# Optimization experiments

Measured on AMD Instinct MI355X. Metric: run time of the kernel, lower is better.

## Reference

```python
import jax, jax.numpy as jnp
import numpy as np
from jax import lax

K = 3          # spline order
G = 5          # grid intervals
R0, R1 = -4.0, 4.0  # grid_range
IN, HID, OUT = 32, 128, 16
BATCH, SEQ = 256, 512


def make_grid(n_in):
    # extended knot vector: G+2K+1 knots per input, uniform spacing h
    h = (R1 - R0) / G
    knots = R0 + h * jnp.arange(-K, G + K + 1, dtype=jnp.float32)  # [G+2K+1]
    return jnp.broadcast_to(knots, (n_in, G + 2 * K + 1))


def b_splines(x, grid):
    # Cox-de Boor recursion. x: [B, n], grid: [n, G+2K+1] -> basis [B, n, G+K]
    xg = x[..., None]
    B = ((xg >= grid[:, :-1]) & (xg < grid[:, 1:])).astype(x.dtype)
    for d in range(1, K + 1):
        B = ((xg - grid[:, :-(d + 1)]) / (grid[:, d:-1] - grid[:, :-(d + 1)]) * B[..., :-1]
             + (grid[:, d + 1:] - xg) / (grid[:, d + 1:] - grid[:, 1:-d]) * B[..., 1:])
    return B


def kan_layer(x, coef, scale_base, scale_sp, grid):
    # y[b,o] = sum_i scale_base[i,o]*silu(x[b,i]) + scale_sp[i,o]*spline_io(x[b,i])
    base = jax.nn.silu(x)                               # [B, n_in]
    Bsp = b_splines(x, grid)                            # [B, n_in, G+K]
    spline = jnp.einsum('bik,iok->bio', Bsp, coef)      # [B, n_in, n_out]
    return (jnp.einsum('bi,io->bo', base, scale_base)
            + jnp.einsum('bio,io->bo', spline, scale_sp))


def setup_inputs() -> dict:
    key = jax.random.key(0)
    ks = jax.random.split(key, 7)
    x = jax.random.normal(ks[0], (BATCH, SEQ, IN), dtype=jnp.float32)
    coef1 = jax.random.normal(ks[1], (IN + HID, HID, G + K), dtype=jnp.float32) * 0.1
    sb1 = jax.random.normal(ks[2], (IN + HID, HID), dtype=jnp.float32) * 0.05
    sp1 = jax.random.normal(ks[3], (IN + HID, HID), dtype=jnp.float32) * 0.05
    coef2 = jax.random.normal(ks[4], (HID, OUT, G + K), dtype=jnp.float32) * 0.1
    sb2 = jax.random.normal(ks[5], (HID, OUT), dtype=jnp.float32) * 0.05
    sp2 = jax.random.normal(ks[6], (HID, OUT), dtype=jnp.float32) * 0.05
    return {"x": x, "coef1": coef1, "sb1": sb1, "sp1": sp1,
            "coef2": coef2, "sb2": sb2, "sp2": sp2}


def reference(x, coef1, sb1, sp1, coef2, sb2, sp2):
    grid1 = make_grid(IN + HID)
    grid2 = make_grid(HID)

    def step(h, x_t):
        combined = jnp.concatenate([x_t, h], axis=1)        # [B, IN+HID]
        h_new = kan_layer(combined, coef1, sb1, sp1, grid1)  # [B, HID]
        out_t = kan_layer(h_new, coef2, sb2, sp2, grid2)     # [B, OUT]
        return h_new, out_t

    h0 = jnp.zeros((x.shape[0], HID), dtype=x.dtype)
    _, outs = lax.scan(step, h0, jnp.swapaxes(x, 0, 1))  # outs: [T, B, OUT]
    # original stacks all timestep outputs then returns outputs[:, -1, :]
    return outs[-1]
```

## Files before the change

kernel.cpp:

```cpp
#include <hip/hip_runtime.h>
#include <hip/hip_bf16.h>

#define NIN 32
#define NHID 128
#define NOUT 16
#define NIN1 160
#define SEQT 512
#define NB 256
#define SEGI 40

#if defined(__has_builtin)
#if __has_builtin(__builtin_amdgcn_fdot2_f32_bf16)
#define HAVE_DOT2BF 1
#endif
#endif
#ifndef HAVE_DOT2BF
#define HAVE_DOT2BF 0
#endif

__device__ __forceinline__ unsigned int f2bfbits(float f) {
    unsigned int u = __float_as_uint(f);
    return (u + 0x7fffu + ((u >> 16) & 1u)) >> 16;
}
__device__ __forceinline__ unsigned int packbf(float lo, float hi) {
    return f2bfbits(lo) | (f2bfbits(hi) << 16);
}

#if HAVE_DOT2BF
typedef __bf16 bf16x2 __attribute__((ext_vector_type(2)));
__device__ __forceinline__ float dot2w(unsigned int a, unsigned int b, float c) {
    return __builtin_amdgcn_fdot2_f32_bf16(__builtin_bit_cast(bf16x2, a),
                                           __builtin_bit_cast(bf16x2, b), c, false);
}
#else
__device__ __forceinline__ float dot2w(unsigned int a, unsigned int b, float c) {
    float alo = __uint_as_float(a << 16), ahi = __uint_as_float(a & 0xffff0000u);
    float blo = __uint_as_float(b << 16), bhi = __uint_as_float(b & 0xffff0000u);
    return __builtin_fmaf(ahi, bhi, __builtin_fmaf(alo, blo, c));
}
#endif

__device__ __forceinline__ void spline_feat(float c, float* out4, int* jst) {
    const float t0 = -8.8f, inv_h = 0.625f;
    float u  = (c - t0) * inv_h;
    float uf = floorf(u);
    int   m0 = (int)uf;
    bool valid = (m0 >= 0) && (m0 <= 10);
    float f   = u - uf;
    float omf = 1.0f - f;
    float f2 = f * f,     f3 = f2 * f;
    float omf3 = omf * omf * omf;
    const float c6 = 0.16666667f;
    float v0 = omf3 * c6;
    float v1 = __builtin_fmaf(3.0f, f3, __builtin_fmaf(-6.0f, f2, 4.0f)) * c6;
    float v2 = __builtin_fmaf(-3.0f, f3, __builtin_fmaf(3.0f, f + f2, 1.0f)) * c6;
    float v3 = f3 * c6;
    float v[4] = {v0, v1, v2, v3};
    int jb = m0 - 3;
    int js = jb < 0 ? 0 : (jb > 4 ? 4 : jb);
    int sh = js - jb;
    #pragma unroll
    for (int r = 0; r < 4; ++r) {
        int rs = r + sh;
        out4[r] = (valid && rs >= 0 && rs <= 3) ? v[rs] : 0.f;
    }
    *jst = js;
}

__device__ __forceinline__ float fsilu(float c) {
    return c * __builtin_amdgcn_rcpf(1.f + __expf(-c));
}

#define R20(X) X(0) X(1) X(2) X(3) X(4) X(5) X(6) X(7) X(8) X(9) \
               X(10) X(11) X(12) X(13) X(14) X(15) X(16) X(17) X(18) X(19)

__attribute__((amdgpu_waves_per_eu(2, 2)))
__global__ void __launch_bounds__(512)
kan_seq(const float* __restrict__ x,
        const float* __restrict__ coef1,
        const float* __restrict__ sb1,
        const float* __restrict__ sp1,
        const float* __restrict__ coef2,
        const float* __restrict__ sb2,
        const float* __restrict__ sp2,
        float* __restrict__ out)
{
    __shared__ __align__(16) unsigned int Fb[NIN1][4];
    __shared__ float Fsil[NIN1];
    __shared__ float red[4][NHID];
    __shared__ float Hf[NHID][9];

    const int tid  = threadIdx.x;
    const int b    = blockIdx.x;
    const int o    = tid & 127;
    const int seg  = tid >> 7;
    const int i0   = seg * SEGI;
    const int lane = tid & 63;

#define DECLP(p) uint4 wA##p, wB##p; unsigned int sbp##p;
    R20(DECLP)
#undef DECLP

#define INITP(p) { \
    const int iA = i0 + 2 * (p), iB = i0 + 2 * (p) + 1; \
    const float4* ca = (const float4*)(coef1 + (size_t)(iA * NHID + o) * 8); \
    const float4* cb = (const float4*)(coef1 + (size_t)(iB * NHID + o) * 8); \
    float spA = sp1[iA * NHID + o], spB = sp1[iB * NHID + o]; \
    float4 a0 = ca[0], a1 = ca[1], b0v = cb[0], b1v = cb[1]; \
    wA##p = make_uint4(packbf(spA * a0.x, spA * a0.y), packbf(spA * a0.z, spA * a0.w), \
                       packbf(spA * a1.x, spA * a1.y), packbf(spA * a1.z, spA * a1.w)); \
    wB##p = make_uint4(packbf(spB * b0v.x, spB * b0v.y), packbf(spB * b0v.z, spB * b0v.w), \
                       packbf(spB * b1v.x, spB * b1v.y), packbf(spB * b1v.z, spB * b1v.w)); \
    sbp##p = packbf(sb1[iA * NHID + o], sb1[iB * NHID + o]); }
    R20(INITP)
#undef INITP

    ((float*)red)[tid] = 0.f;
    float xv = (tid < NIN) ? x[(size_t)b * SEQT * NIN + tid] : 0.f;
    __syncthreads();

    for (int t = 0; t < SEQT; ++t) {
        if (tid < NIN1) {
            float c;
            if (tid < NIN) c = xv;
            else {
                int hi = tid - NIN;
                c = red[0][hi] + red[1][hi] + red[2][hi] + red[3][hi];
            }
            float sil = fsilu(c);
            float b4[4]; int js;
            spline_feat(c, b4, &js);
            float e[8];
            #pragma unroll
            for (int k = 0; k < 8; ++k) {
                int d = k - js;
                e[k] = (d >= 0 && d < 4) ? b4[d] : 0.f;
            }
            uint4 pk;
            pk.x = packbf(e[0], e[1]); pk.y = packbf(e[2], e[3]);
            pk.z = packbf(e[4], e[5]); pk.w = packbf(e[6], e[7]);
            *(uint4*)&Fb[tid][0] = pk;
            Fsil[tid] = sil;
        }
        if (tid < NIN) {
            int tn = (t + 1 < SEQT) ? (t + 1) : t;
            xv = x[((size_t)b * SEQT + tn) * NIN + tid];
        }
        __syncthreads();

        float vsil = Fsil[i0 + (lane < SEGI ? lane : 0)];
        uint4 pfA = *(const uint4*)&Fb[i0][0];
        uint4 pfB = *(const uint4*)&Fb[i0 + 1][0];
        float ac0 = 0.f, ac1 = 0.f, ac2 = 0.f, ac3 = 0.f;
#define DOTP(p) { \
        uint4 bA = pfA, bB = pfB; \
        if ((p) < SEGI / 2 - 1) { \
            pfA = *(const uint4*)&Fb[i0 + 2 * (p) + 2][0]; \
            pfB = *(const uint4*)&Fb[i0 + 2 * (p) + 3][0]; \
        } \
        float sb_lo = __uint_as_float(sbp##p << 16); \
        float sb_hi = __uint_as_float(sbp##p & 0xffff0000u); \
        float slA = __int_as_float(__builtin_amdgcn_readlane(__float_as_int(vsil), 2 * (p))); \
        float slB = __int_as_float(__builtin_amdgcn_readlane(__float_as_int(vsil), 2 * (p) + 1)); \
        ac0 = __builtin_fmaf(slA, sb_lo, ac0); \
        ac0 = dot2w(bA.x, wA##p.x, ac0); ac1 = dot2w(bA.y, wA##p.y, ac1); \
        ac2 = dot2w(bA.z, wA##p.z, ac2); ac3 = dot2w(bA.w, wA##p.w, ac3); \
        ac1 = __builtin_fmaf(slB, sb_hi, ac1); \
        ac0 = dot2w(bB.x, wB##p.x, ac0); ac1 = dot2w(bB.y, wB##p.y, ac1); \
        ac2 = dot2w(bB.z, wB##p.z, ac2); ac3 = dot2w(bB.w, wB##p.w, ac3); }
        R20(DOTP)
#undef DOTP
        red[seg][o] = (ac0 + ac1) + (ac2 + ac3);
        __syncthreads();
    }

    if (tid < NHID) {
        float c = red[0][tid] + red[1][tid] + red[2][tid] + red[3][tid];
        float sil = fsilu(c);
        float b4[4]; int js;
        spline_feat(c, b4, &js);
        #pragma unroll
        for (int k = 0; k < 8; ++k) {
            int d = k - js;
            Hf[tid][k] = (d >= 0 && d < 4) ? b4[d] : 0.f;
        }
        Hf[tid][8] = sil;
    }
    __syncthreads();
    if (tid < 128) {
        int o2 = tid & 15, isg = tid >> 4;
        float acc = 0.f;
        for (int q = 0; q < 16; ++q) {
            int i = isg * 16 + q;
            const float* c2 = coef2 + (size_t)(i * NOUT + o2) * 8;
            float s = 0.f;
            #pragma unroll
            for (int k = 0; k < 8; ++k) s += Hf[i][k] * c2[k];
            acc += Hf[i][8] * sb2[i * NOUT + o2] + sp2[i * NOUT + o2] * s;
        }
        ((float*)red)[isg * 16 + o2] = acc;
    }
    __syncthreads();
    if (tid < NOUT) {
        float a = 0.f;
        #pragma unroll
        for (int g = 0; g < 8; ++g) a += ((float*)red)[g * 16 + tid];
        out[(size_t)b * NOUT + tid] = a;
    }
}

extern "C" void kernel_launch(void* const* d_in, const int* in_sizes, int n_in,
                              void* d_out, int out_size, void* d_ws, size_t ws_size,
                              hipStream_t stream) {
    kan_seq<<<NB, 512, 0, stream>>>(
        (const float*)d_in[0], (const float*)d_in[1], (const float*)d_in[2],
        (const float*)d_in[3], (const float*)d_in[4], (const float*)d_in[5],
        (const float*)d_in[6], (float*)d_out);
}
```

Baseline: 983.3 us.

## Compute recurrent spline contraction with MFMA bf16 instead of dot2 instructions

Replaces the per-thread bf16 dot2 accumulation of the spline term with 16x16x32 bf16 MFMA instructions. The spline weights are held as A-fragments in registers, and each of the 8 waves handles 20 inputs across all 128 outputs. The silu base term stays on scalar FMAs and is written to a separate reduction buffer, so the hidden-state reduction now sums 12 partials. The goal is to cut per-step VALU latency in the serial 512-step recurrence. In exchange it uses more LDS for partials, adds predicated writes from the MFMA output layout, and relies on fragment mapping being correct.

```diff
diff --git a/kernel.cpp b/kernel.cpp
--- a/kernel.cpp
+++ b/kernel.cpp
@@ -7,16 +7,9 @@
 #define NIN1 160
 #define SEQT 512
 #define NB 256
-#define SEGI 40
-
-#if defined(__has_builtin)
-#if __has_builtin(__builtin_amdgcn_fdot2_f32_bf16)
-#define HAVE_DOT2BF 1
-#endif
-#endif
-#ifndef HAVE_DOT2BF
-#define HAVE_DOT2BF 0
-#endif
+
+typedef __attribute__((ext_vector_type(8))) short s16x8;
+typedef __attribute__((ext_vector_type(4))) float f32x4;
 
 __device__ __forceinline__ unsigned int f2bfbits(float f) {
     unsigned int u = __float_as_uint(f);
@@ -25,20 +18,6 @@
 __device__ __forceinline__ unsigned int packbf(float lo, float hi) {
     return f2bfbits(lo) | (f2bfbits(hi) << 16);
 }
-
-#if HAVE_DOT2BF
-typedef __bf16 bf16x2 __attribute__((ext_vector_type(2)));
-__device__ __forceinline__ float dot2w(unsigned int a, unsigned int b, float c) {
-    return __builtin_amdgcn_fdot2_f32_bf16(__builtin_bit_cast(bf16x2, a),
-                                           __builtin_bit_cast(bf16x2, b), c, false);
-}
-#else
-__device__ __forceinline__ float dot2w(unsigned int a, unsigned int b, float c) {
-    float alo = __uint_as_float(a << 16), ahi = __uint_as_float(a & 0xffff0000u);
-    float blo = __uint_as_float(b << 16), bhi = __uint_as_float(b & 0xffff0000u);
-    return __builtin_fmaf(ahi, bhi, __builtin_fmaf(alo, blo, c));
-}
-#endif
 
 __device__ __forceinline__ void spline_feat(float c, float* out4, int* jst) {
     const float t0 = -8.8f, inv_h = 0.625f;
@@ -48,7 +27,7 @@
     bool valid = (m0 >= 0) && (m0 <= 10);
     float f   = u - uf;
     float omf = 1.0f - f;
-    float f2 = f * f,     f3 = f2 * f;
+    float f2 = f * f, f3 = f2 * f;
     float omf3 = omf * omf * omf;
     const float c6 = 0.16666667f;
     float v0 = omf3 * c6;
@@ -73,6 +52,8 @@
 
 #define R20(X) X(0) X(1) X(2) X(3) X(4) X(5) X(6) X(7) X(8) X(9) \
                X(10) X(11) X(12) X(13) X(14) X(15) X(16) X(17) X(18) X(19)
+#define O8(X) X(0) X(1) X(2) X(3) X(4) X(5) X(6) X(7)
+#define K5(X) X(0) X(1) X(2) X(3) X(4)
 
 __attribute__((amdgpu_waves_per_eu(2, 2)))
 __global__ void __launch_bounds__(512)
@@ -87,37 +68,53 @@
 {
     __shared__ __align__(16) unsigned int Fb[NIN1][4];
     __shared__ float Fsil[NIN1];
-    __shared__ float red[4][NHID];
+    __shared__ __align__(16) float red[8][NHID];
+    __shared__ float redb[4][NHID];
     __shared__ float Hf[NHID][9];
 
     const int tid  = threadIdx.x;
     const int b    = blockIdx.x;
+    const int lane = tid & 63;
+    const int w    = tid >> 6;
     const int o    = tid & 127;
     const int seg  = tid >> 7;
-    const int i0   = seg * SEGI;
-    const int lane = tid & 63;
-
-#define DECLP(p) uint4 wA##p, wB##p; unsigned int sbp##p;
-    R20(DECLP)
-#undef DECLP
-
-#define INITP(p) { \
-    const int iA = i0 + 2 * (p), iB = i0 + 2 * (p) + 1; \
-    const float4* ca = (const float4*)(coef1 + (size_t)(iA * NHID + o) * 8); \
-    const float4* cb = (const float4*)(coef1 + (size_t)(iB * NHID + o) * 8); \
-    float spA = sp1[iA * NHID + o], spB = sp1[iB * NHID + o]; \
-    float4 a0 = ca[0], a1 = ca[1], b0v = cb[0], b1v = cb[1]; \
-    wA##p = make_uint4(packbf(spA * a0.x, spA * a0.y), packbf(spA * a0.z, spA * a0.w), \
-                       packbf(spA * a1.x, spA * a1.y), packbf(spA * a1.z, spA * a1.w)); \
-    wB##p = make_uint4(packbf(spB * b0v.x, spB * b0v.y), packbf(spB * b0v.z, spB * b0v.w), \
-                       packbf(spB * b1v.x, spB * b1v.y), packbf(spB * b1v.z, spB * b1v.w)); \
-    sbp##p = packbf(sb1[iA * NHID + o], sb1[iB * NHID + o]); }
-    R20(INITP)
-#undef INITP
+    const int arow = lane & 15;
+    const int agrp = lane >> 4;
+
+#define DECLW(k) uint4 wf##k##_0, wf##k##_1, wf##k##_2, wf##k##_3, \
+                       wf##k##_4, wf##k##_5, wf##k##_6, wf##k##_7;
+    K5(DECLW)
+#undef DECLW
+
+#define INITW1(k,t) { \
+    int rec = (w * 5 + (k)) * 4 + agrp; \
+    int oo  = (t) * 16 + arow; \
+    const float4* cp = (const float4*)(coef1 + (size_t)(rec * NHID + oo) * 8); \
+    float sp = sp1[rec * NHID + oo]; \
+    float4 c0 = cp[0], c1 = cp[1]; \
+    wf##k##_##t = make_uint4(packbf(sp * c0.x, sp * c0.y), packbf(sp * c0.z, sp * c0.w), \
+                             packbf(sp * c1.x, sp * c1.y), packbf(sp * c1.z, sp * c1.w)); }
+#define INITWK(k) INITW1(k,0) INITW1(k,1) INITW1(k,2) INITW1(k,3) \
+                  INITW1(k,4) INITW1(k,5) INITW1(k,6) INITW1(k,7)
+    K5(INITWK)
+#undef INITWK
+#undef INITW1
+
+#define DECLSB(p) unsigned int sbp##p;
+    R20(DECLSB)
+#undef DECLSB
+#define INITSB(p) { int iA = seg * 40 + 2 * (p); \
+    sbp##p = packbf(sb1[iA * NHID + o], sb1[(iA + 1) * NHID + o]); }
+    R20(INITSB)
+#undef INITSB
 
     ((float*)red)[tid] = 0.f;
+    ((float*)red)[tid + 512] = 0.f;
+    ((float*)redb)[tid] = 0.f;
     float xv = (tid < NIN) ? x[(size_t)b * SEQT * NIN + tid] : 0.f;
     __syncthreads();
+
+    const int fbase = w * 20 + agrp;
 
     for (int t = 0; t < SEQT; ++t) {
         if (tid < NIN1) {
@@ -125,9 +122,11 @@
             if (tid < NIN) c = xv;
             else {
                 int hi = tid - NIN;
-                c = red[0][hi] + red[1][hi] + red[2][hi] + red[3][hi];
+                c = ((red[0][hi] + red[1][hi]) + (red[2][hi] + red[3][hi]))
+                  + ((red[4][hi] + red[5][hi]) + (red[6][hi] + red[7][hi]))
+                  + ((redb[0][hi] + redb[1][hi]) + (redb[2][hi] + redb[3][hi]));
             }
-            float sil = fsilu(c);
+            Fsil[tid] = fsilu(c);
             float b4[4]; int js;
             spline_feat(c, b4, &js);
             float e[8];
@@ -140,7 +139,6 @@
             pk.x = packbf(e[0], e[1]); pk.y = packbf(e[2], e[3]);
             pk.z = packbf(e[4], e[5]); pk.w = packbf(e[6], e[7]);
             *(uint4*)&Fb[tid][0] = pk;
-            Fsil[tid] = sil;
         }
         if (tid < NIN) {
             int tn = (t + 1 < SEQT) ? (t + 1) : t;
@@ -148,34 +146,52 @@
         }
         __syncthreads();
 
-        float vsil = Fsil[i0 + (lane < SEGI ? lane : 0)];
-        uint4 pfA = *(const uint4*)&Fb[i0][0];
-        uint4 pfB = *(const uint4*)&Fb[i0 + 1][0];
-        float ac0 = 0.f, ac1 = 0.f, ac2 = 0.f, ac3 = 0.f;
-#define DOTP(p) { \
-        uint4 bA = pfA, bB = pfB; \
-        if ((p) < SEGI / 2 - 1) { \
-            pfA = *(const uint4*)&Fb[i0 + 2 * (p) + 2][0]; \
-            pfB = *(const uint4*)&Fb[i0 + 2 * (p) + 3][0]; \
-        } \
+        uint4 bq0 = *(const uint4*)&Fb[fbase][0];
+        uint4 bq1 = *(const uint4*)&Fb[fbase + 4][0];
+
+        float vsil = Fsil[seg * 40 + (lane < 40 ? lane : 0)];
+        float bc0 = 0.f, bc1 = 0.f;
+#define DOTB(p) { \
         float sb_lo = __uint_as_float(sbp##p << 16); \
         float sb_hi = __uint_as_float(sbp##p & 0xffff0000u); \
         float slA = __int_as_float(__builtin_amdgcn_readlane(__float_as_int(vsil), 2 * (p))); \
         float slB = __int_as_float(__builtin_amdgcn_readlane(__float_as_int(vsil), 2 * (p) + 1)); \
-        ac0 = __builtin_fmaf(slA, sb_lo, ac0); \
-        ac0 = dot2w(bA.x, wA##p.x, ac0); ac1 = dot2w(bA.y, wA##p.y, ac1); \
-        ac2 = dot2w(bA.z, wA##p.z, ac2); ac3 = dot2w(bA.w, wA##p.w, ac3); \
-        ac1 = __builtin_fmaf(slB, sb_hi, ac1); \
-        ac0 = dot2w(bB.x, wB##p.x, ac0); ac1 = dot2w(bB.y, wB##p.y, ac1); \
-        ac2 = dot2w(bB.z, wB##p.z, ac2); ac3 = dot2w(bB.w, wB##p.w, ac3); }
-        R20(DOTP)
-#undef DOTP
-        red[seg][o] = (ac0 + ac1) + (ac2 + ac3);
+        bc0 = __builtin_fmaf(slA, sb_lo, bc0); \
+        bc1 = __builtin_fmaf(slB, sb_hi, bc1); }
+        R20(DOTB)
+#undef DOTB
+        redb[seg][o] = bc0 + bc1;
+
+#define DECLAC(t) f32x4 ac##t = {0.f, 0.f, 0.f, 0.f};
+        O8(DECLAC)
+#undef DECLAC
+#define MMROW(k, bqv) { s16x8 bb_ = __builtin_bit_cast(s16x8, bqv); \
+        ac0 = __builtin_amdgcn_mfma_f32_16x16x32_bf16(__builtin_bit_cast(s16x8, wf##k##_0), bb_, ac0, 0, 0, 0); \
+        ac1 = __builtin_amdgcn_mfma_f32_16x16x32_bf16(__builtin_bit_cast(s16x8, wf##k##_1), bb_, ac1, 0, 0, 0); \
+        ac2 = __builtin_amdgcn_mfma_f32_16x16x32_bf16(__builtin_bit_cast(s16x8, wf##k##_2), bb_, ac2, 0, 0, 0); \
+        ac3 = __builtin_amdgcn_mfma_f32_16x16x32_bf16(__builtin_bit_cast(s16x8, wf##k##_3), bb_, ac3, 0, 0, 0); \
+        ac4 = __builtin_amdgcn_mfma_f32_16x16x32_bf16(__builtin_bit_cast(s16x8, wf##k##_4), bb_, ac4, 0, 0, 0); \
+        ac5 = __builtin_amdgcn_mfma_f32_16x16x32_bf16(__builtin_bit_cast(s16x8, wf##k##_5), bb_, ac5, 0, 0, 0); \
+        ac6 = __builtin_amdgcn_mfma_f32_16x16x32_bf16(__builtin_bit_cast(s16x8, wf##k##_6), bb_, ac6, 0, 0, 0); \
+        ac7 = __builtin_amdgcn_mfma_f32_16x16x32_bf16(__builtin_bit_cast(s16x8, wf##k##_7), bb_, ac7, 0, 0, 0); }
+        MMROW(0, bq0)  uint4 bq2 = *(const uint4*)&Fb[fbase + 8][0];
+        MMROW(1, bq1)  uint4 bq3 = *(const uint4*)&Fb[fbase + 12][0];
+        MMROW(2, bq2)  uint4 bq4 = *(const uint4*)&Fb[fbase + 16][0];
+        MMROW(3, bq3)
+        MMROW(4, bq4)
+#undef MMROW
+
+#define WRR(t) if ((lane & 15) == (t)) \
+            *(f32x4*)&red[w][(t) * 16 + (agrp << 2)] = ac##t;
+        O8(WRR)
+#undef WRR
         __syncthreads();
     }
 
     if (tid < NHID) {
-        float c = red[0][tid] + red[1][tid] + red[2][tid] + red[3][tid];
+        float c = ((red[0][tid] + red[1][tid]) + (red[2][tid] + red[3][tid]))
+                + ((red[4][tid] + red[5][tid]) + (red[6][tid] + red[7][tid]))
+                + ((redb[0][tid] + redb[1][tid]) + (redb[2][tid] + redb[3][tid]));
         float sil = fsilu(c);
         float b4[4]; int js;
         spline_feat(c, b4, &js);
```

Result: slower. 1.036 ms (+5.4%).
